# Kernel optimization log

Hardware: AMD Instinct MI355X
Metric: run time of the kernel (lower is better)

Reference implementation:

```python
import jax, jax.numpy as jnp
import numpy as np

B, T, D_IN, H = 1024, 512, 32, 64


def setup_inputs() -> dict:
    key = jax.random.key(0)
    ks = jax.random.split(key, 9)
    s_in = 1.0 / np.sqrt(D_IN)
    s_h = 1.0 / np.sqrt(H)
    return {
        "X": jax.random.normal(ks[0], (B, T, D_IN), dtype=jnp.float32),
        # embed Linear(D_IN -> H), torch layout [out, in]
        "W_emb": jax.random.uniform(ks[1], (H, D_IN), jnp.float32, -s_in, s_in),
        "b_emb": jax.random.uniform(ks[2], (H,), jnp.float32, -s_in, s_in),
        # RNN weights: weight_ih [H,H], weight_hh [H,H], biases [H]
        "W_ih": jax.random.uniform(ks[3], (H, H), jnp.float32, -s_h, s_h),
        "b_ih": jax.random.uniform(ks[4], (H,), jnp.float32, -s_h, s_h),
        "W_hh": jax.random.uniform(ks[5], (H, H), jnp.float32, -s_h, s_h),
        "b_hh": jax.random.uniform(ks[6], (H,), jnp.float32, -s_h, s_h),
        # output Linear(H -> 1)
        "W_out": jax.random.uniform(ks[7], (1, H), jnp.float32, -s_h, s_h),
        "b_out": jax.random.uniform(ks[8], (1,), jnp.float32, -s_h, s_h),
    }


def reference(X, W_emb, b_emb, W_ih, b_ih, W_hh, b_hh, W_out, b_out):
    # embed: [B,T,D_IN] -> [B,T,H]
    emb = jnp.einsum('btd,hd->bth', X, W_emb) + b_emb
    # precompute input-to-hidden contribution for all steps (big GEMM)
    pre = jnp.einsum('bth,gh->btg', emb, W_ih) + b_ih  # [B,T,H]
    h0 = jnp.zeros((X.shape[0], W_hh.shape[0]), dtype=X.dtype)

    def step(h, x_t):
        # torch RNN (tanh): h' = tanh(x W_ih^T + b_ih + h W_hh^T + b_hh)
        h_new = jnp.tanh(x_t + h @ W_hh.T + b_hh)
        return h_new, None

    hT, _ = jax.lax.scan(step, h0, jnp.swapaxes(pre, 0, 1))  # scan over T
    # final FC on last hidden state -> [B]
    return (hT @ W_out.T + b_out)[:, 0]
```

## Files before the change

kernel.cpp:

```cpp
#include <hip/hip_runtime.h>

#define B_DIM 1024
#define T_DIM 512
#define D_IN 32
#define H 64
#define CT 32
#define NCHUNK (T_DIM / CT)

__global__ __launch_bounds__(1024) void prep_kernel(
    const float* __restrict__ W_emb,
    const float* __restrict__ b_emb,
    const float* __restrict__ W_ih,
    const float* __restrict__ b_ih,
    const float* __restrict__ b_hh,
    float* __restrict__ Wc,
    float* __restrict__ cvec)
{
    const int tid = threadIdx.x;
    const int i  = tid >> 4;
    const int dg = tid & 15;
    float s0 = 0.f, s1 = 0.f;
    #pragma unroll
    for (int j = 0; j < H; ++j) {
        const float w = W_ih[i * H + j];
        s0 += w * W_emb[j * D_IN + dg];
        s1 += w * W_emb[j * D_IN + dg + 16];
    }
    Wc[i * D_IN + dg]      = s0;
    Wc[i * D_IN + dg + 16] = s1;
    if (dg == 0) {
        float s = b_ih[i] + b_hh[i];
        #pragma unroll
        for (int j = 0; j < H; ++j) s += W_ih[i * H + j] * b_emb[j];
        cvec[i] = s;
    }
}

__global__ __launch_bounds__(64) void rnn_kernel(
    const float* __restrict__ X,
    const float* __restrict__ W_hh,
    const float* __restrict__ Wc,
    const float* __restrict__ cvec,
    const float* __restrict__ W_out,
    const float* __restrict__ b_out,
    float* __restrict__ out)
{
    __shared__ __align__(16) float xs[2][CT * D_IN];
    __shared__ __align__(16) float hs[H];

    const int b = blockIdx.x;
    const int i = threadIdx.x;

    float whh[H];
    #pragma unroll
    for (int j = 0; j < H; j += 4) {
        const float4 v = *(const float4*)&W_hh[i * H + j];
        whh[j] = v.x; whh[j + 1] = v.y; whh[j + 2] = v.z; whh[j + 3] = v.w;
    }
    float wc[D_IN];
    #pragma unroll
    for (int d = 0; d < D_IN; d += 4) {
        const float4 v = *(const float4*)&Wc[i * D_IN + d];
        wc[d] = v.x; wc[d + 1] = v.y; wc[d + 2] = v.z; wc[d + 3] = v.w;
    }
    const float ci = cvec[i];

    const float* __restrict__ xb = X + (size_t)b * T_DIM * D_IN;

    {
        float4 st[4];
        #pragma unroll
        for (int k = 0; k < 4; ++k) st[k] = *(const float4*)&xb[k * 256 + i * 4];
        #pragma unroll
        for (int k = 0; k < 4; ++k) *(float4*)&xs[0][k * 256 + i * 4] = st[k];
    }
    hs[i] = 0.f;
    float hlast = 0.f;

    #pragma unroll 1
    for (int c = 0; c < NCHUNK; ++c) {
        const int cur = c & 1;
        float4 pf[4];
        if (c + 1 < NCHUNK) {
            #pragma unroll
            for (int k = 0; k < 4; ++k)
                pf[k] = *(const float4*)&xb[(c + 1) * (CT * D_IN) + k * 256 + i * 4];
        }

        #pragma unroll 2
        for (int tt = 0; tt < CT; ++tt) {
            const float* __restrict__ xrow = &xs[cur][tt * D_IN];
            float a0 = ci, a1 = 0.f, a2 = 0.f, a3 = 0.f;
            #pragma unroll
            for (int d = 0; d < D_IN; d += 4) {
                const float4 xv = *(const float4*)&xrow[d];
                a0 += wc[d]     * xv.x;
                a1 += wc[d + 1] * xv.y;
                a2 += wc[d + 2] * xv.z;
                a3 += wc[d + 3] * xv.w;
            }
            #pragma unroll
            for (int j = 0; j < H; j += 4) {
                const float4 hv = *(const float4*)&hs[j];
                a0 += whh[j]     * hv.x;
                a1 += whh[j + 1] * hv.y;
                a2 += whh[j + 2] * hv.z;
                a3 += whh[j + 3] * hv.w;
            }
            const float acc = (a0 + a1) + (a2 + a3);
            const float e  = __builtin_amdgcn_exp2f(acc * 2.885390081777927f);
            const float hn = __builtin_fmaf(-2.f, __builtin_amdgcn_rcpf(e + 1.f), 1.f);
            hs[i] = hn;
            hlast = hn;
        }

        if (c + 1 < NCHUNK) {
            const int nxt = cur ^ 1;
            #pragma unroll
            for (int k = 0; k < 4; ++k)
                *(float4*)&xs[nxt][k * 256 + i * 4] = pf[k];
        }
    }

    float val = hlast * W_out[i];
    #pragma unroll
    for (int off = 32; off > 0; off >>= 1)
        val += __shfl_xor(val, off, 64);
    if (i == 0) out[b] = val + b_out[0];
}

extern "C" void kernel_launch(void* const* d_in, const int* in_sizes, int n_in,
                              void* d_out, int out_size, void* d_ws, size_t ws_size,
                              hipStream_t stream) {
    const float* X     = (const float*)d_in[0];
    const float* W_emb = (const float*)d_in[1];
    const float* b_emb = (const float*)d_in[2];
    const float* W_ih  = (const float*)d_in[3];
    const float* b_ih  = (const float*)d_in[4];
    const float* W_hh  = (const float*)d_in[5];
    const float* b_hh  = (const float*)d_in[6];
    const float* W_out = (const float*)d_in[7];
    const float* b_out = (const float*)d_in[8];
    float* out = (float*)d_out;

    float* Wc   = (float*)d_ws;
    float* cvec = (float*)d_ws + H * D_IN;

    prep_kernel<<<1, 1024, 0, stream>>>(W_emb, b_emb, W_ih, b_ih, b_hh, Wc, cvec);
    rnn_kernel<<<B_DIM, 64, 0, stream>>>(X, W_hh, Wc, cvec, W_out, b_out, out);
}
```

Baseline: 312.3 us.

## Broadcast hidden state via readlane and fold weight prep into RNN kernel

The hidden state is no longer exchanged through shared memory. It stays in a register, and each step reads the other lanes' values with readlane broadcasts, removing the LDS write/read round trip from the serial recurrence. The separate prep kernel is removed and each block recomputes the combined embedding/input weights and bias itself, eliminating one launch at the cost of redundant per-block setup work. Accumulation now uses 8 partial sums, the kernel is pinned to one wave per EU, and asm barriers keep the weights in VGPRs. Together these raise register pressure and add 64 scalar readlanes per step.

Result: faster. 283.6 us (-9.2%).

```diff
diff --git a/kernel.cpp b/kernel.cpp
--- a/kernel.cpp
+++ b/kernel.cpp
@@ -7,49 +7,64 @@
 #define CT 32
 #define NCHUNK (T_DIM / CT)
 
-__global__ __launch_bounds__(1024) void prep_kernel(
+__global__ __attribute__((amdgpu_flat_work_group_size(64, 64),
+                          amdgpu_waves_per_eu(1, 1)))
+void rnn_kernel(
+    const float* __restrict__ X,
     const float* __restrict__ W_emb,
     const float* __restrict__ b_emb,
     const float* __restrict__ W_ih,
     const float* __restrict__ b_ih,
+    const float* __restrict__ W_hh,
     const float* __restrict__ b_hh,
-    float* __restrict__ Wc,
-    float* __restrict__ cvec)
-{
-    const int tid = threadIdx.x;
-    const int i  = tid >> 4;
-    const int dg = tid & 15;
-    float s0 = 0.f, s1 = 0.f;
-    #pragma unroll
-    for (int j = 0; j < H; ++j) {
-        const float w = W_ih[i * H + j];
-        s0 += w * W_emb[j * D_IN + dg];
-        s1 += w * W_emb[j * D_IN + dg + 16];
-    }
-    Wc[i * D_IN + dg]      = s0;
-    Wc[i * D_IN + dg + 16] = s1;
-    if (dg == 0) {
-        float s = b_ih[i] + b_hh[i];
-        #pragma unroll
-        for (int j = 0; j < H; ++j) s += W_ih[i * H + j] * b_emb[j];
-        cvec[i] = s;
-    }
-}
-
-__global__ __launch_bounds__(64) void rnn_kernel(
-    const float* __restrict__ X,
-    const float* __restrict__ W_hh,
-    const float* __restrict__ Wc,
-    const float* __restrict__ cvec,
     const float* __restrict__ W_out,
     const float* __restrict__ b_out,
     float* __restrict__ out)
 {
+    __shared__ __align__(16) float wemb[H * D_IN];
+    __shared__ __align__(16) float bemb[H];
     __shared__ __align__(16) float xs[2][CT * D_IN];
-    __shared__ __align__(16) float hs[H];
 
     const int b = blockIdx.x;
     const int i = threadIdx.x;
+
+    const float* __restrict__ xb = X + (size_t)b * T_DIM * D_IN;
+
+    float4 st0, st1, st2, st3;
+    st0 = *(const float4*)&xb[0 * 256 + i * 4];
+    st1 = *(const float4*)&xb[1 * 256 + i * 4];
+    st2 = *(const float4*)&xb[2 * 256 + i * 4];
+    st3 = *(const float4*)&xb[3 * 256 + i * 4];
+
+    #pragma unroll
+    for (int k = 0; k < 8; ++k)
+        *(float4*)&wemb[k * 256 + i * 4] = *(const float4*)&W_emb[k * 256 + i * 4];
+    bemb[i] = b_emb[i];
+
+    float wih[H];
+    #pragma unroll
+    for (int j = 0; j < H; j += 4) {
+        const float4 v = *(const float4*)&W_ih[i * H + j];
+        wih[j] = v.x; wih[j + 1] = v.y; wih[j + 2] = v.z; wih[j + 3] = v.w;
+    }
+
+    float wc[D_IN];
+    #pragma unroll
+    for (int d = 0; d < D_IN; ++d) wc[d] = 0.f;
+    float ci = b_ih[i] + b_hh[i];
+    #pragma unroll 4
+    for (int j = 0; j < H; ++j) {
+        const float wj = wih[j];
+        ci += wj * bemb[j];
+        #pragma unroll
+        for (int d = 0; d < D_IN; d += 4) {
+            const float4 e = *(const float4*)&wemb[j * D_IN + d];
+            wc[d]     += wj * e.x;
+            wc[d + 1] += wj * e.y;
+            wc[d + 2] += wj * e.z;
+            wc[d + 3] += wj * e.w;
+        }
+    }
 
     float whh[H];
     #pragma unroll
@@ -57,72 +72,90 @@
         const float4 v = *(const float4*)&W_hh[i * H + j];
         whh[j] = v.x; whh[j + 1] = v.y; whh[j + 2] = v.z; whh[j + 3] = v.w;
     }
-    float wc[D_IN];
+
     #pragma unroll
-    for (int d = 0; d < D_IN; d += 4) {
-        const float4 v = *(const float4*)&Wc[i * D_IN + d];
-        wc[d] = v.x; wc[d + 1] = v.y; wc[d + 2] = v.z; wc[d + 3] = v.w;
-    }
-    const float ci = cvec[i];
+    for (int j = 0; j < H; ++j) asm volatile("" : "+v"(whh[j]));
+    #pragma unroll
+    for (int d = 0; d < D_IN; ++d) asm volatile("" : "+v"(wc[d]));
+    asm volatile("" : "+v"(ci));
 
-    const float* __restrict__ xb = X + (size_t)b * T_DIM * D_IN;
+    *(float4*)&xs[0][0 * 256 + i * 4] = st0;
+    *(float4*)&xs[0][1 * 256 + i * 4] = st1;
+    *(float4*)&xs[0][2 * 256 + i * 4] = st2;
+    *(float4*)&xs[0][3 * 256 + i * 4] = st3;
 
-    {
-        float4 st[4];
-        #pragma unroll
-        for (int k = 0; k < 4; ++k) st[k] = *(const float4*)&xb[k * 256 + i * 4];
-        #pragma unroll
-        for (int k = 0; k < 4; ++k) *(float4*)&xs[0][k * 256 + i * 4] = st[k];
-    }
-    hs[i] = 0.f;
-    float hlast = 0.f;
+    float h = 0.f;
 
     #pragma unroll 1
     for (int c = 0; c < NCHUNK; ++c) {
         const int cur = c & 1;
-        float4 pf[4];
+        float4 pf0, pf1, pf2, pf3;
         if (c + 1 < NCHUNK) {
-            #pragma unroll
-            for (int k = 0; k < 4; ++k)
-                pf[k] = *(const float4*)&xb[(c + 1) * (CT * D_IN) + k * 256 + i * 4];
+            const float* __restrict__ nb = &xb[(c + 1) * (CT * D_IN)];
+            pf0 = *(const float4*)&nb[0 * 256 + i * 4];
+            pf1 = *(const float4*)&nb[1 * 256 + i * 4];
+            pf2 = *(const float4*)&nb[2 * 256 + i * 4];
+            pf3 = *(const float4*)&nb[3 * 256 + i * 4];
         }
 
         #pragma unroll 2
         for (int tt = 0; tt < CT; ++tt) {
             const float* __restrict__ xrow = &xs[cur][tt * D_IN];
-            float a0 = ci, a1 = 0.f, a2 = 0.f, a3 = 0.f;
+
+            const float4 x0 = *(const float4*)&xrow[0];
+            const float4 x1 = *(const float4*)&xrow[4];
+            const float4 x2 = *(const float4*)&xrow[8];
+            const float4 x3 = *(const float4*)&xrow[12];
+            const float4 x4 = *(const float4*)&xrow[16];
+            const float4 x5 = *(const float4*)&xrow[20];
+            const float4 x6 = *(const float4*)&xrow[24];
+            const float4 x7 = *(const float4*)&xrow[28];
+
+            float a[8];
+            a[0] = ci;
             #pragma unroll
-            for (int d = 0; d < D_IN; d += 4) {
-                const float4 xv = *(const float4*)&xrow[d];
-                a0 += wc[d]     * xv.x;
-                a1 += wc[d + 1] * xv.y;
-                a2 += wc[d + 2] * xv.z;
-                a3 += wc[d + 3] * xv.w;
+            for (int k = 1; k < 8; ++k) a[k] = 0.f;
+
+            const int hb = __float_as_int(h);
+            #pragma unroll
+            for (int j = 0; j < H; ++j) {
+                const float hj = __int_as_float(__builtin_amdgcn_readlane(hb, j));
+                a[j & 7] += whh[j] * hj;
             }
-            #pragma unroll
-            for (int j = 0; j < H; j += 4) {
-                const float4 hv = *(const float4*)&hs[j];
-                a0 += whh[j]     * hv.x;
-                a1 += whh[j + 1] * hv.y;
-                a2 += whh[j + 2] * hv.z;
-                a3 += whh[j + 3] * hv.w;
-            }
-            const float acc = (a0 + a1) + (a2 + a3);
+
+            a[0] += wc[0]  * x0.x;  a[1] += wc[1]  * x0.y;
+            a[2] += wc[2]  * x0.z;  a[3] += wc[3]  * x0.w;
+            a[4] += wc[4]  * x1.x;  a[5] += wc[5]  * x1.y;
+            a[6] += wc[6]  * x1.z;  a[7] += wc[7]  * x1.w;
+            a[0] += wc[8]  * x2.x;  a[1] += wc[9]  * x2.y;
+            a[2] += wc[10] * x2.z;  a[3] += wc[11] * x2.w;
+            a[4] += wc[12] * x3.x;  a[5] += wc[13] * x3.y;
+            a[6] += wc[14] * x3.z;  a[7] += wc[15] * x3.w;
+            a[0] += wc[16] * x4.x;  a[1] += wc[17] * x4.y;
+            a[2] += wc[18] * x4.z;  a[3] += wc[19] * x4.w;
+            a[4] += wc[20] * x5.x;  a[5] += wc[21] * x5.y;
+            a[6] += wc[22] * x5.z;  a[7] += wc[23] * x5.w;
+            a[0] += wc[24] * x6.x;  a[1] += wc[25] * x6.y;
+            a[2] += wc[26] * x6.z;  a[3] += wc[27] * x6.w;
+            a[4] += wc[28] * x7.x;  a[5] += wc[29] * x7.y;
+            a[6] += wc[30] * x7.z;  a[7] += wc[31] * x7.w;
+
+            const float acc = ((a[0] + a[1]) + (a[2] + a[3]))
+                            + ((a[4] + a[5]) + (a[6] + a[7]));
             const float e  = __builtin_amdgcn_exp2f(acc * 2.885390081777927f);
-            const float hn = __builtin_fmaf(-2.f, __builtin_amdgcn_rcpf(e + 1.f), 1.f);
-            hs[i] = hn;
-            hlast = hn;
+            h = __builtin_fmaf(-2.f, __builtin_amdgcn_rcpf(e + 1.f), 1.f);
         }
 
         if (c + 1 < NCHUNK) {
             const int nxt = cur ^ 1;
-            #pragma unroll
-            for (int k = 0; k < 4; ++k)
-                *(float4*)&xs[nxt][k * 256 + i * 4] = pf[k];
+            *(float4*)&xs[nxt][0 * 256 + i * 4] = pf0;
+            *(float4*)&xs[nxt][1 * 256 + i * 4] = pf1;
+            *(float4*)&xs[nxt][2 * 256 + i * 4] = pf2;
+            *(float4*)&xs[nxt][3 * 256 + i * 4] = pf3;
         }
     }
 
-    float val = hlast * W_out[i];
+    float val = h * W_out[i];
     #pragma unroll
     for (int off = 32; off > 0; off >>= 1)
         val += __shfl_xor(val, off, 64);
@@ -143,9 +176,6 @@
     const float* b_out = (const float*)d_in[8];
     float* out = (float*)d_out;
 
-    float* Wc   = (float*)d_ws;
-    float* cvec = (float*)d_ws + H * D_IN;
-
-    prep_kernel<<<1, 1024, 0, stream>>>(W_emb, b_emb, W_ih, b_ih, b_hh, Wc, cvec);
-    rnn_kernel<<<B_DIM, 64, 0, stream>>>(X, W_hh, Wc, cvec, W_out, b_out, out);
+    rnn_kernel<<<B_DIM, 64, 0, stream>>>(X, W_emb, b_emb, W_ih, b_ih,
+                                         W_hh, b_hh, W_out, b_out, out);
 }
```
